# Performance work log

Measured on AMD Instinct MI355X. Metric: run time of the kernel, lower is better.

The kernel has to match this reference:

```python
import jax, jax.numpy as jnp
import numpy as np

C, HEADS, H, W = 256, 8, 64, 64
HD = C // HEADS
EPS = 1e-5

def conv1x1(x, w, b):
    # x:[B,C,H,W], w:[O,C], b:[O]
    return jnp.einsum('bchw,oc->bohw', x, w) + b[None, :, None, None]

def group_norm(x, scale, bias):
    B = x.shape[0]
    xg = x.reshape(B, HEADS, HD, H, W)
    mu = jnp.mean(xg, axis=(2, 3, 4), keepdims=True)
    var = jnp.var(xg, axis=(2, 3, 4), keepdims=True)
    xn = ((xg - mu) * jax.lax.rsqrt(var + EPS)).reshape(B, C, H, W)
    return xn * scale[None, :, None, None] + bias[None, :, None, None]

def setup_inputs() -> dict:
    key = jax.random.key(0)
    ks = jax.random.split(key, 12)
    s = 1.0 / np.sqrt(C)
    d = {
        'x': jax.random.normal(ks[0], (1, C, H, W), jnp.float32),
        'wq': jax.random.normal(ks[1], (C, C), jnp.float32) * s,
        'bq': jax.random.normal(ks[2], (C,), jnp.float32) * 0.01,
        'wk': jax.random.normal(ks[3], (C, C), jnp.float32) * s,
        'bk': jax.random.normal(ks[4], (C,), jnp.float32) * 0.01,
        'wv': jax.random.normal(ks[5], (C, C), jnp.float32) * s,
        'bv': jax.random.normal(ks[6], (C,), jnp.float32) * 0.01,
        'wo': jax.random.normal(ks[7], (C, C), jnp.float32) * s,
        'bo': jax.random.normal(ks[8], (C,), jnp.float32) * 0.01,
        'gn_scale': jnp.ones((C,), jnp.float32),
        'gn_bias': jnp.zeros((C,), jnp.float32),
        'gamma': jax.random.normal(ks[9], (1,), jnp.float32) * 0.1,
    }
    return d

def reference(x, wq, bq, wk, bk, wv, bv, wo, bo, gn_scale, gn_bias, gamma):
    B = x.shape[0]
    N = H * W
    scale = HD ** (-0.5)
    xn = group_norm(x, gn_scale, gn_bias)
    q = conv1x1(xn, wq, bq).reshape(B, HEADS, HD, N)
    k = conv1x1(xn, wk, bk).reshape(B, HEADS, HD, N)
    v = conv1x1(xn, wv, bv).reshape(B, HEADS, HD, N)
    attn = jnp.einsum('bhdn,bhdm->bhnm', q, k) * scale  # [B,h,N,N]
    attn = jax.nn.softmax(attn, axis=-1)
    out = jnp.einsum('bhnm,bhdm->bhdn', attn, v).reshape(B, C, H, W)
    out = conv1x1(out, wo, bo)
    return x + gamma * out
```

## Files before the change

kernel.cpp:

```cpp
#include <hip/hip_runtime.h>
#include <hip/hip_bf16.h>

#define C_DIM 256
#define N_SP  4096
#define HEADS 8
#define HD    32
#define GSIZE (HD * N_SP)

typedef __attribute__((ext_vector_type(8))) short bf16x8;
typedef __attribute__((ext_vector_type(4))) float f32x4;
typedef __attribute__((ext_vector_type(4))) unsigned u32x4;

__device__ inline unsigned short f2bf(float f) {
  unsigned int u = __builtin_bit_cast(unsigned int, f);
  u = (u + 0x7fffu + ((u >> 16) & 1u)) >> 16;
  return (unsigned short)u;
}
__device__ inline float bf2f(unsigned short b) {
  return __builtin_bit_cast(float, (unsigned)b << 16);
}

__device__ inline unsigned cvtpk_bf16(float lo, float hi) {
  unsigned r;
  asm("v_cvt_pk_bf16_f32 %0, %1, %2" : "=v"(r) : "v"(lo), "v"(hi));
  return r;
}
__device__ inline void pl32swap(unsigned &x, unsigned &y) {
  asm("v_permlane32_swap_b32 %0, %1" : "+v"(x), "+v"(y));
}
__device__ inline void pl16swap(unsigned &x, unsigned &y) {
  asm("v_permlane16_swap_b32 %0, %1" : "+v"(x), "+v"(y));
}
__device__ inline void gload_lds16(const void* g, void* l) {
  __builtin_amdgcn_global_load_lds(
      (const __attribute__((address_space(1))) void*)g,
      (__attribute__((address_space(3))) void*)l, 16, 0, 0);
}

__global__ __launch_bounds__(1024) void stats_cvt(const float* __restrict__ x,
                                                  float* __restrict__ stats,
                                                  const float* __restrict__ wq,
                                                  const float* __restrict__ wk,
                                                  const float* __restrict__ wv,
                                                  const float* __restrict__ wo,
                                                  unsigned short* __restrict__ dst) {
  int t = threadIdx.x;
  if (blockIdx.x < 8) {
    int g = blockIdx.x;
    const float4* xg = reinterpret_cast<const float4*>(x + (size_t)g * GSIZE);
    float s1 = 0.f, s2 = 0.f;
#pragma unroll
    for (int i = 0; i < 32; ++i) {
      float4 v = xg[t + i * 1024];
      s1 += v.x + v.y + v.z + v.w;
      s2 += v.x * v.x + v.y * v.y + v.z * v.z + v.w * v.w;
    }
    for (int off = 1; off < 64; off <<= 1) {
      s1 += __shfl_xor(s1, off);
      s2 += __shfl_xor(s2, off);
    }
    __shared__ float red[16][2];
    int wid = t >> 6;
    if ((t & 63) == 0) { red[wid][0] = s1; red[wid][1] = s2; }
    __syncthreads();
    if (t < 16) {
      s1 = red[t][0]; s2 = red[t][1];
      for (int off = 1; off < 16; off <<= 1) {
        s1 += __shfl_xor(s1, off);
        s2 += __shfl_xor(s2, off);
      }
      if (t == 0) {
        float mu = s1 / (float)GSIZE;
        float var = s2 / (float)GSIZE - mu * mu;
        stats[g * 2] = mu;
        stats[g * 2 + 1] = rsqrtf(var + 1e-5f);
      }
    }
  } else {
    int i = (blockIdx.x - 8) * 1024 + t;
    int mat = i >> 14;
    int idx = i & 16383;
    const float* src = (mat == 0) ? wq : (mat == 1) ? wk : (mat == 2) ? wv : wo;
    float4 v = reinterpret_cast<const float4*>(src)[idx];
    ushort4 o;
    o.x = f2bf(v.x); o.y = f2bf(v.y); o.z = f2bf(v.z); o.w = f2bf(v.w);
    reinterpret_cast<ushort4*>(dst + (size_t)mat * 65536)[idx] = o;
  }
}

__global__ __launch_bounds__(256) void gn_apply_t(const float* __restrict__ x,
                                                  const float* __restrict__ stats,
                                                  const float* __restrict__ gsc,
                                                  const float* __restrict__ gbi,
                                                  unsigned short* __restrict__ xnt) {
  __shared__ float tile[64][65];
  int t = threadIdx.x;
  int p0 = blockIdx.x * 64;
  int c0 = blockIdx.y * 64;
#pragma unroll
  for (int pass = 0; pass < 4; ++pass) {
    int f = t + pass * 256;
    int row = f >> 4, f4 = f & 15;
    int c = c0 + row;
    float4 v = *reinterpret_cast<const float4*>(x + (size_t)c * N_SP + p0 + f4 * 4);
    float mu = stats[(c >> 5) * 2], rs = stats[(c >> 5) * 2 + 1];
    float sc = gsc[c] * rs;
    float bi = gbi[c] - mu * sc;
    tile[row][f4 * 4 + 0] = v.x * sc + bi;
    tile[row][f4 * 4 + 1] = v.y * sc + bi;
    tile[row][f4 * 4 + 2] = v.z * sc + bi;
    tile[row][f4 * 4 + 3] = v.w * sc + bi;
  }
  __syncthreads();
#pragma unroll
  for (int pass = 0; pass < 4; ++pass) {
    int f = t + pass * 256;
    int p = f >> 4, cg = f & 15;
    ushort4 o;
    o.x = f2bf(tile[cg * 4 + 0][p]);
    o.y = f2bf(tile[cg * 4 + 1][p]);
    o.z = f2bf(tile[cg * 4 + 2][p]);
    o.w = f2bf(tile[cg * 4 + 3][p]);
    *reinterpret_cast<ushort4*>(xnt + (size_t)(p0 + p) * C_DIM + c0 + cg * 4) = o;
  }
}

__global__ __launch_bounds__(256) void gemm_qkv(const unsigned short* __restrict__ xnt,
                                                const unsigned short* __restrict__ wbf,
                                                const float* __restrict__ bq,
                                                const float* __restrict__ bk,
                                                const float* __restrict__ bv,
                                                unsigned short* __restrict__ qt,
                                                unsigned short* __restrict__ kt,
                                                unsigned short* __restrict__ vv) {
  int t = threadIdx.x;
  int w = t >> 6, lc = t & 15, lg = (t & 63) >> 4;
  int z = blockIdx.y;
  const unsigned short* Wb = wbf + (size_t)z * 65536;

  if (z < 2) {
    const float* bias = (z == 0) ? bq : bk;
    unsigned short* outt = (z == 0) ? qt : kt;
    float scale = (z == 0) ? 0.25503344494963116f : 1.0f;
    int n_base = (blockIdx.x >> 1) * 32 + (w >> 1) * 16;
    int o_base = (blockIdx.x & 1) * 128 + (w & 1) * 64;
    f32x4 acc[4];
#pragma unroll
    for (int ni = 0; ni < 4; ++ni) acc[ni] = (f32x4){0.f, 0.f, 0.f, 0.f};
#pragma unroll
    for (int c0 = 0; c0 < 256; c0 += 32) {
      bf16x8 a = *reinterpret_cast<const bf16x8*>(
          xnt + (size_t)(n_base + lc) * C_DIM + c0 + 8 * lg);
#pragma unroll
      for (int ni = 0; ni < 4; ++ni) {
        bf16x8 b = *reinterpret_cast<const bf16x8*>(
            Wb + (size_t)(o_base + 16 * ni + lc) * C_DIM + c0 + 8 * lg);
        acc[ni] = __builtin_amdgcn_mfma_f32_16x16x32_bf16(a, b, acc[ni], 0, 0, 0);
      }
    }
#pragma unroll
    for (int ni = 0; ni < 4; ++ni) {
      float bvv = bias[o_base + 16 * ni + lc];
#pragma unroll
      for (int r = 0; r < 4; ++r)
        outt[(size_t)(n_base + 4 * lg + r) * C_DIM + o_base + 16 * ni + lc] =
            f2bf((acc[ni][r] + bvv) * scale);
    }
  } else {
    int o_base = (blockIdx.x >> 6) * 64 + (w >> 1) * 32;
    int p_base = (blockIdx.x & 63) * 64 + (w & 1) * 32;
    f32x4 acc[2][2];
#pragma unroll
    for (int mi = 0; mi < 2; ++mi)
#pragma unroll
      for (int ni = 0; ni < 2; ++ni) acc[mi][ni] = (f32x4){0.f, 0.f, 0.f, 0.f};
#pragma unroll
    for (int c0 = 0; c0 < 256; c0 += 32) {
      bf16x8 a[2], b[2];
#pragma unroll
      for (int mi = 0; mi < 2; ++mi)
        a[mi] = *reinterpret_cast<const bf16x8*>(
            Wb + (size_t)(o_base + 16 * mi + lc) * C_DIM + c0 + 8 * lg);
#pragma unroll
      for (int ni = 0; ni < 2; ++ni)
        b[ni] = *reinterpret_cast<const bf16x8*>(
            xnt + (size_t)(p_base + 16 * ni + lc) * C_DIM + c0 + 8 * lg);
#pragma unroll
      for (int mi = 0; mi < 2; ++mi)
#pragma unroll
        for (int ni = 0; ni < 2; ++ni)
          acc[mi][ni] = __builtin_amdgcn_mfma_f32_16x16x32_bf16(a[mi], b[ni], acc[mi][ni], 0, 0, 0);
    }
#pragma unroll
    for (int mi = 0; mi < 2; ++mi)
#pragma unroll
      for (int r = 0; r < 4; ++r) {
        int o = o_base + 16 * mi + 4 * lg + r;
        float bvv = bv[o];
#pragma unroll
        for (int ni = 0; ni < 2; ++ni)
          vv[(size_t)o * N_SP + p_base + 16 * ni + lc] = f2bf(acc[mi][ni][r] + bvv);
      }
  }
}


#define STAGE_T(KB, VB, IT)                                                   \
  {                                                                           \
    gload_lds16(ksrc + (size_t)(IT) * 32768, smem + (KB) + w1024);            \
    gload_lds16(vsrc + (size_t)(IT) * 128, smem + (VB) + w1024);              \
  }

#define COMPUTE_TILE_L(KB, VB)                                                \
  {                                                                           \
    bf16x8 kf[4];                                                             \
    _Pragma("unroll")                                                         \
    for (int ni = 0; ni < 4; ++ni)                                            \
      kf[ni] = *reinterpret_cast<const bf16x8*>(smem + (KB) + ni * 1024 + krd); \
    bf16x8 vf[2][2];                                                          \
    _Pragma("unroll")                                                         \
    for (int dd = 0; dd < 2; ++dd) {                                          \
      vf[0][dd] = *reinterpret_cast<const bf16x8*>(smem + (VB) + dd * 2048 + vrd0); \
      vf[1][dd] = *reinterpret_cast<const bf16x8*>(smem + (VB) + dd * 2048 + vrd1); \
    }                                                                         \
    _Pragma("unroll")                                                         \
    for (int qi = 0; qi < 4; ++qi) {                                          \
      f32x4 s[4];                                                             \
      _Pragma("unroll")                                                       \
      for (int ni = 0; ni < 4; ++ni) {                                        \
        f32x4 z = (f32x4){0.f, 0.f, 0.f, 0.f};                                \
        s[ni] = __builtin_amdgcn_mfma_f32_16x16x32_bf16(kf[ni], qf[qi], z, 0, 0, 0); \
      }                                                                       \
      unsigned wd[4][2];                                                      \
      _Pragma("unroll")                                                       \
      for (int ni = 0; ni < 4; ++ni) {                                        \
        float p0 = __builtin_amdgcn_exp2f(s[ni][0]);                          \
        float p1 = __builtin_amdgcn_exp2f(s[ni][1]);                          \
        float p2 = __builtin_amdgcn_exp2f(s[ni][2]);                          \
        float p3 = __builtin_amdgcn_exp2f(s[ni][3]);                          \
        wd[ni][0] = cvtpk_bf16(p0, p1);                                       \
        wd[ni][1] = cvtpk_bf16(p2, p3);                                       \
      }                                                                       \
      bf16x8 ap[2];                                                           \
      _Pragma("unroll")                                                       \
      for (int kk = 0; kk < 2; ++kk) {                                        \
        unsigned a0 = wd[2 * kk][0], b0 = wd[2 * kk + 1][0];                  \
        unsigned a1 = wd[2 * kk][1], b1 = wd[2 * kk + 1][1];                  \
        pl32swap(a0, b0); pl16swap(a0, b0);                                   \
        pl32swap(a1, b1); pl16swap(a1, b1);                                   \
        u32x4 pk = {a0, a1, b0, b1};                                          \
        ap[kk] = __builtin_bit_cast(bf16x8, pk);                              \
      }                                                                       \
      lacc[qi] = __builtin_amdgcn_mfma_f32_16x16x32_bf16(ap[0], ones, lacc[qi], 0, 0, 0); \
      oacc[qi][0] = __builtin_amdgcn_mfma_f32_16x16x32_bf16(ap[0], vf[0][0], oacc[qi][0], 0, 0, 0); \
      oacc[qi][1] = __builtin_amdgcn_mfma_f32_16x16x32_bf16(ap[0], vf[0][1], oacc[qi][1], 0, 0, 0); \
      lacc[qi] = __builtin_amdgcn_mfma_f32_16x16x32_bf16(ap[1], ones, lacc[qi], 0, 0, 0); \
      oacc[qi][0] = __builtin_amdgcn_mfma_f32_16x16x32_bf16(ap[1], vf[1][0], oacc[qi][0], 0, 0, 0); \
      oacc[qi][1] = __builtin_amdgcn_mfma_f32_16x16x32_bf16(ap[1], vf[1][1], oacc[qi][1], 0, 0, 0); \
    }                                                                         \
  }

#define SYNC_T                                                                \
  {                                                                           \
    asm volatile("s_waitcnt vmcnt(0)" ::: "memory");                          \
    __syncthreads();                                                          \
  }

__global__ __launch_bounds__(256) void attn_part(const unsigned short* __restrict__ qt,
                                                 const unsigned short* __restrict__ kt,
                                                 const unsigned short* __restrict__ v,
                                                 unsigned short* __restrict__ po,
                                                 float* __restrict__ lp) {
  __shared__ __align__(1024) char smem[16384];
  int t = threadIdx.x;
  int w = t >> 6, lane = t & 63, lc = t & 15, lg = (t & 63) >> 4;
  int h = blockIdx.y, ks = blockIdx.z;
  int hc = h * HD;
  int nq0 = blockIdx.x * 256 + w * 64;
  int w1024 = w << 10;

  int kg = 64 * w + lane;
  int krow = kg >> 2;
  int kc16 = (kg & 3) ^ (krow & 3);
  const char* ksrc = (const char*)(kt + (size_t)(ks * 1024 + krow) * C_DIM + hc + 8 * kc16);
  int vg = 64 * w + lane;
  int vrow = vg >> 3;
  int vn16 = (vg & 7) ^ (vrow & 7);
  const char* vsrc = (const char*)(v + (size_t)(hc + vrow) * N_SP + ks * 1024 + 8 * vn16);

  int krd = lc * 64 + 16 * (lg ^ (lc & 3));
  int vrd0 = lc * 128 + 16 * ((lg + 0) ^ (lc & 7));
  int vrd1 = lc * 128 + 16 * ((lg + 4) ^ (lc & 7));

  bf16x8 qf[4];
#pragma unroll
  for (int qi = 0; qi < 4; ++qi)
    qf[qi] = *reinterpret_cast<const bf16x8*>(
        qt + (size_t)(nq0 + 16 * qi + lc) * C_DIM + hc + 8 * lg);

  f32x4 oacc[4][2], lacc[4];
#pragma unroll
  for (int qi = 0; qi < 4; ++qi) {
    lacc[qi] = (f32x4){0.f, 0.f, 0.f, 0.f};
#pragma unroll
    for (int dd = 0; dd < 2; ++dd) oacc[qi][dd] = (f32x4){0.f, 0.f, 0.f, 0.f};
  }
  const bf16x8 ones = {0x3F80, 0x3F80, 0x3F80, 0x3F80, 0x3F80, 0x3F80, 0x3F80, 0x3F80};

  STAGE_T(0, 8192, 0)
  SYNC_T
  for (int p = 0; p < 7; ++p) {
    STAGE_T(4096, 12288, 2 * p + 1)
    COMPUTE_TILE_L(0, 8192)
    SYNC_T
    STAGE_T(0, 8192, 2 * p + 2)
    COMPUTE_TILE_L(4096, 12288)
    SYNC_T
  }
  STAGE_T(4096, 12288, 15)
  COMPUTE_TILE_L(0, 8192)
  SYNC_T
  COMPUTE_TILE_L(4096, 12288)

  unsigned short* pob = po + (size_t)ks * (N_SP * C_DIM);
#pragma unroll
  for (int qi = 0; qi < 4; ++qi)
#pragma unroll
    for (int dd = 0; dd < 2; ++dd)
#pragma unroll
      for (int r = 0; r < 4; ++r)
        pob[(size_t)(nq0 + 16 * qi + 4 * lg + r) * C_DIM + hc + 16 * dd + lc] =
            f2bf(oacc[qi][dd][r]);
  if (lc == 0) {
#pragma unroll
    for (int qi = 0; qi < 4; ++qi)
#pragma unroll
      for (int r = 0; r < 4; ++r)
        lp[ks * 32768 + h * N_SP + nq0 + 16 * qi + 4 * lg + r] = lacc[qi][r];
  }
}

__global__ __launch_bounds__(256) void attn_merge(const unsigned short* __restrict__ po,
                                                  const float* __restrict__ lp,
                                                  unsigned short* __restrict__ aot) {
  int i = blockIdx.x * 256 + threadIdx.x;
  int n = i >> 5;
  int c0 = (i & 31) * 8;
  int h = c0 >> 5;
  float l = lp[h * N_SP + n] + lp[32768 + h * N_SP + n] +
            lp[65536 + h * N_SP + n] + lp[98304 + h * N_SP + n];
  float rl = 1.0f / l;
  float acc[8] = {0.f, 0.f, 0.f, 0.f, 0.f, 0.f, 0.f, 0.f};
#pragma unroll
  for (int ksplit = 0; ksplit < 4; ++ksplit) {
    bf16x8 vv = *reinterpret_cast<const bf16x8*>(po + (size_t)ksplit * (N_SP * C_DIM) + (size_t)i * 8);
#pragma unroll
    for (int j = 0; j < 8; ++j) acc[j] += bf2f((unsigned short)vv[j]);
  }
  bf16x8 o;
#pragma unroll
  for (int j = 0; j < 8; ++j) o[j] = (short)f2bf(acc[j] * rl);
  *reinterpret_cast<bf16x8*>(aot + (size_t)i * 8) = o;
}

__global__ __launch_bounds__(256) void gemm_out(const unsigned short* __restrict__ Wb,
                                                const unsigned short* __restrict__ aot,
                                                const float* __restrict__ bias,
                                                const float* __restrict__ x,
                                                const float* __restrict__ gamma,
                                                float* __restrict__ out) {
  int t = threadIdx.x;
  int w = t >> 6, lc = t & 15, lg = (t & 63) >> 4;
  int o_base = blockIdx.y * 64 + (w >> 1) * 32;
  int p_base = blockIdx.x * 64 + (w & 1) * 32;
  f32x4 acc[2][2];
#pragma unroll
  for (int mi = 0; mi < 2; ++mi)
#pragma unroll
    for (int ni = 0; ni < 2; ++ni) acc[mi][ni] = (f32x4){0.f, 0.f, 0.f, 0.f};
#pragma unroll
  for (int c0 = 0; c0 < 256; c0 += 32) {
    bf16x8 a[2], b[2];
#pragma unroll
    for (int mi = 0; mi < 2; ++mi)
      a[mi] = *reinterpret_cast<const bf16x8*>(
          Wb + (size_t)(o_base + 16 * mi + lc) * C_DIM + c0 + 8 * lg);
#pragma unroll
    for (int ni = 0; ni < 2; ++ni)
      b[ni] = *reinterpret_cast<const bf16x8*>(
          aot + (size_t)(p_base + 16 * ni + lc) * C_DIM + c0 + 8 * lg);
#pragma unroll
    for (int mi = 0; mi < 2; ++mi)
#pragma unroll
      for (int ni = 0; ni < 2; ++ni)
        acc[mi][ni] = __builtin_amdgcn_mfma_f32_16x16x32_bf16(a[mi], b[ni], acc[mi][ni], 0, 0, 0);
  }
  float g = gamma[0];
#pragma unroll
  for (int mi = 0; mi < 2; ++mi)
#pragma unroll
    for (int r = 0; r < 4; ++r) {
      int o = o_base + 16 * mi + 4 * lg + r;
      float bvv = bias[o];
#pragma unroll
      for (int ni = 0; ni < 2; ++ni) {
        size_t idx = (size_t)o * N_SP + p_base + 16 * ni + lc;
        out[idx] = x[idx] + g * (acc[mi][ni][r] + bvv);
      }
    }
}

extern "C" void kernel_launch(void* const* d_in, const int* in_sizes, int n_in,
                              void* d_out, int out_size, void* d_ws, size_t ws_size,
                              hipStream_t stream) {
  const float* x   = (const float*)d_in[0];
  const float* wq  = (const float*)d_in[1];
  const float* bq  = (const float*)d_in[2];
  const float* wk  = (const float*)d_in[3];
  const float* bk  = (const float*)d_in[4];
  const float* wv  = (const float*)d_in[5];
  const float* bv  = (const float*)d_in[6];
  const float* wo  = (const float*)d_in[7];
  const float* bo  = (const float*)d_in[8];
  const float* gsc = (const float*)d_in[9];
  const float* gbi = (const float*)d_in[10];
  const float* gamma = (const float*)d_in[11];
  float* out = (float*)d_out;

  char* ws = (char*)d_ws;
  float* stats          = (float*)ws;
  unsigned short* wbf   = (unsigned short*)(ws + 1024);
  unsigned short* qt    = (unsigned short*)(ws + 525312);
  unsigned short* kt    = (unsigned short*)(ws + 2622464);
  unsigned short* vv    = (unsigned short*)(ws + 4719616);
  unsigned short* aot   = (unsigned short*)(ws + 6816768);
  float* lp             = (float*)(ws + 8913920);
  unsigned short* xnt   = (unsigned short*)(ws + 9962496);
  unsigned short* po    = (unsigned short*)(ws + 12059648);

  stats_cvt<<<72, 1024, 0, stream>>>(x, stats, wq, wk, wv, wo, wbf);
  gn_apply_t<<<dim3(64, 4), 256, 0, stream>>>(x, stats, gsc, gbi, xnt);
  gemm_qkv<<<dim3(256, 3), 256, 0, stream>>>(xnt, wbf, bq, bk, bv, qt, kt, vv);
  attn_part<<<dim3(16, 8, 4), 256, 0, stream>>>(qt, kt, vv, po, lp);
  attn_merge<<<512, 256, 0, stream>>>(po, lp, aot);
  gemm_out<<<dim3(64, 4), 256, 0, stream>>>(wbf + 3 * 65536, aot, bo, x, gamma, out);
}
```

Measured before the change: 75.07 us.

## Double key tile per pipeline stage and interleave two independent MFMA chains

Each pipeline stage of the attention kernel now stages two 64-key K/V sub-tiles into a doubled 32 KB LDS buffer, which halves the number of barrier/waitcnt synchronisations per block. Inside each query sub-block it runs two independent score→exp→PV chains back to back so the scheduler can overlap MFMA latency with exp and permute work. Launch bounds now request 2 blocks per CU. In exchange the kernel uses more registers and LDS, which may reduce occupancy.

```diff
diff --git a/kernel.cpp b/kernel.cpp
--- a/kernel.cpp
+++ b/kernel.cpp
@@ -205,58 +205,69 @@
 }
 
 
-#define STAGE_T(KB, VB, IT)                                                   \
+#define STAGE_P(BB, IT)                                                       \
   {                                                                           \
-    gload_lds16(ksrc + (size_t)(IT) * 32768, smem + (KB) + w1024);            \
-    gload_lds16(vsrc + (size_t)(IT) * 128, smem + (VB) + w1024);              \
-  }
-
-#define COMPUTE_TILE_L(KB, VB)                                                \
+    gload_lds16(ksrc + (size_t)(IT) * 65536, smem + (BB) + w1024);            \
+    gload_lds16(ksrc + (size_t)(IT) * 65536 + 32768, smem + (BB) + 4096 + w1024); \
+    gload_lds16(vsrc + (size_t)(IT) * 256, smem + (BB) + 8192 + w1024);       \
+    gload_lds16(vsrc + (size_t)(IT) * 256 + 128, smem + (BB) + 12288 + w1024);\
+  }
+
+#define CHAIN(KF, VF)                                                         \
   {                                                                           \
-    bf16x8 kf[4];                                                             \
-    _Pragma("unroll")                                                         \
-    for (int ni = 0; ni < 4; ++ni)                                            \
-      kf[ni] = *reinterpret_cast<const bf16x8*>(smem + (KB) + ni * 1024 + krd); \
-    bf16x8 vf[2][2];                                                          \
+    f32x4 s[4];                                                               \
+    _Pragma("unroll")                                                         \
+    for (int ni = 0; ni < 4; ++ni) {                                          \
+      f32x4 z = (f32x4){0.f, 0.f, 0.f, 0.f};                                  \
+      s[ni] = __builtin_amdgcn_mfma_f32_16x16x32_bf16(KF[ni], qf[qi], z, 0, 0, 0); \
+    }                                                                         \
+    unsigned wd[4][2];                                                        \
+    _Pragma("unroll")                                                         \
+    for (int ni = 0; ni < 4; ++ni) {                                          \
+      float p0 = __builtin_amdgcn_exp2f(s[ni][0]);                            \
+      float p1 = __builtin_amdgcn_exp2f(s[ni][1]);                            \
+      float p2 = __builtin_amdgcn_exp2f(s[ni][2]);                            \
+      float p3 = __builtin_amdgcn_exp2f(s[ni][3]);                            \
+      wd[ni][0] = cvtpk_bf16(p0, p1);                                         \
+      wd[ni][1] = cvtpk_bf16(p2, p3);                                         \
+    }                                                                         \
+    bf16x8 ap[2];                                                             \
+    _Pragma("unroll")                                                         \
+    for (int kk = 0; kk < 2; ++kk) {                                          \
+      unsigned a0 = wd[2 * kk][0], b0 = wd[2 * kk + 1][0];                    \
+      unsigned a1 = wd[2 * kk][1], b1 = wd[2 * kk + 1][1];                    \
+      pl32swap(a0, b0); pl16swap(a0, b0);                                     \
+      pl32swap(a1, b1); pl16swap(a1, b1);                                     \
+      u32x4 pk = {a0, a1, b0, b1};                                            \
+      ap[kk] = __builtin_bit_cast(bf16x8, pk);                                \
+    }                                                                         \
+    lacc[qi] = __builtin_amdgcn_mfma_f32_16x16x32_bf16(ap[0], ones, lacc[qi], 0, 0, 0); \
+    oacc[qi][0] = __builtin_amdgcn_mfma_f32_16x16x32_bf16(ap[0], VF[0][0], oacc[qi][0], 0, 0, 0); \
+    oacc[qi][1] = __builtin_amdgcn_mfma_f32_16x16x32_bf16(ap[0], VF[0][1], oacc[qi][1], 0, 0, 0); \
+    lacc[qi] = __builtin_amdgcn_mfma_f32_16x16x32_bf16(ap[1], ones, lacc[qi], 0, 0, 0); \
+    oacc[qi][0] = __builtin_amdgcn_mfma_f32_16x16x32_bf16(ap[1], VF[1][0], oacc[qi][0], 0, 0, 0); \
+    oacc[qi][1] = __builtin_amdgcn_mfma_f32_16x16x32_bf16(ap[1], VF[1][1], oacc[qi][1], 0, 0, 0); \
+  }
+
+#define COMPUTE_P(BB)                                                         \
+  {                                                                           \
+    bf16x8 kf0[4], kf1[4], vf0[2][2], vf1[2][2];                              \
+    _Pragma("unroll")                                                         \
+    for (int ni = 0; ni < 4; ++ni) {                                          \
+      kf0[ni] = *reinterpret_cast<const bf16x8*>(smem + (BB) + ni * 1024 + krd); \
+      kf1[ni] = *reinterpret_cast<const bf16x8*>(smem + (BB) + 4096 + ni * 1024 + krd); \
+    }                                                                         \
     _Pragma("unroll")                                                         \
     for (int dd = 0; dd < 2; ++dd) {                                          \
-      vf[0][dd] = *reinterpret_cast<const bf16x8*>(smem + (VB) + dd * 2048 + vrd0); \
-      vf[1][dd] = *reinterpret_cast<const bf16x8*>(smem + (VB) + dd * 2048 + vrd1); \
+      vf0[0][dd] = *reinterpret_cast<const bf16x8*>(smem + (BB) + 8192 + dd * 2048 + vrd0); \
+      vf0[1][dd] = *reinterpret_cast<const bf16x8*>(smem + (BB) + 8192 + dd * 2048 + vrd1); \
+      vf1[0][dd] = *reinterpret_cast<const bf16x8*>(smem + (BB) + 12288 + dd * 2048 + vrd0); \
+      vf1[1][dd] = *reinterpret_cast<const bf16x8*>(smem + (BB) + 12288 + dd * 2048 + vrd1); \
     }                                                                         \
     _Pragma("unroll")                                                         \
     for (int qi = 0; qi < 4; ++qi) {                                          \
-      f32x4 s[4];                                                             \
-      _Pragma("unroll")                                                       \
-      for (int ni = 0; ni < 4; ++ni) {                                        \
-        f32x4 z = (f32x4){0.f, 0.f, 0.f, 0.f};                                \
-        s[ni] = __builtin_amdgcn_mfma_f32_16x16x32_bf16(kf[ni], qf[qi], z, 0, 0, 0); \
-      }                                                                       \
-      unsigned wd[4][2];                                                      \
-      _Pragma("unroll")                                                       \
-      for (int ni = 0; ni < 4; ++ni) {                                        \
-        float p0 = __builtin_amdgcn_exp2f(s[ni][0]);                          \
-        float p1 = __builtin_amdgcn_exp2f(s[ni][1]);                          \
-        float p2 = __builtin_amdgcn_exp2f(s[ni][2]);                          \
-        float p3 = __builtin_amdgcn_exp2f(s[ni][3]);                          \
-        wd[ni][0] = cvtpk_bf16(p0, p1);                                       \
-        wd[ni][1] = cvtpk_bf16(p2, p3);                                       \
-      }                                                                       \
-      bf16x8 ap[2];                                                           \
-      _Pragma("unroll")                                                       \
-      for (int kk = 0; kk < 2; ++kk) {                                        \
-        unsigned a0 = wd[2 * kk][0], b0 = wd[2 * kk + 1][0];                  \
-        unsigned a1 = wd[2 * kk][1], b1 = wd[2 * kk + 1][1];                  \
-        pl32swap(a0, b0); pl16swap(a0, b0);                                   \
-        pl32swap(a1, b1); pl16swap(a1, b1);                                   \
-        u32x4 pk = {a0, a1, b0, b1};                                          \
-        ap[kk] = __builtin_bit_cast(bf16x8, pk);                              \
-      }                                                                       \
-      lacc[qi] = __builtin_amdgcn_mfma_f32_16x16x32_bf16(ap[0], ones, lacc[qi], 0, 0, 0); \
-      oacc[qi][0] = __builtin_amdgcn_mfma_f32_16x16x32_bf16(ap[0], vf[0][0], oacc[qi][0], 0, 0, 0); \
-      oacc[qi][1] = __builtin_amdgcn_mfma_f32_16x16x32_bf16(ap[0], vf[0][1], oacc[qi][1], 0, 0, 0); \
-      lacc[qi] = __builtin_amdgcn_mfma_f32_16x16x32_bf16(ap[1], ones, lacc[qi], 0, 0, 0); \
-      oacc[qi][0] = __builtin_amdgcn_mfma_f32_16x16x32_bf16(ap[1], vf[1][0], oacc[qi][0], 0, 0, 0); \
-      oacc[qi][1] = __builtin_amdgcn_mfma_f32_16x16x32_bf16(ap[1], vf[1][1], oacc[qi][1], 0, 0, 0); \
+      CHAIN(kf0, vf0)                                                         \
+      CHAIN(kf1, vf1)                                                         \
     }                                                                         \
   }
 
@@ -266,12 +277,12 @@
     __syncthreads();                                                          \
   }
 
-__global__ __launch_bounds__(256) void attn_part(const unsigned short* __restrict__ qt,
-                                                 const unsigned short* __restrict__ kt,
-                                                 const unsigned short* __restrict__ v,
-                                                 unsigned short* __restrict__ po,
-                                                 float* __restrict__ lp) {
-  __shared__ __align__(1024) char smem[16384];
+__global__ __launch_bounds__(256, 2) void attn_part(const unsigned short* __restrict__ qt,
+                                                    const unsigned short* __restrict__ kt,
+                                                    const unsigned short* __restrict__ v,
+                                                    unsigned short* __restrict__ po,
+                                                    float* __restrict__ lp) {
+  __shared__ __align__(1024) char smem[32768];
   int t = threadIdx.x;
   int w = t >> 6, lane = t & 63, lc = t & 15, lg = (t & 63) >> 4;
   int h = blockIdx.y, ks = blockIdx.z;
@@ -307,20 +318,20 @@
   }
   const bf16x8 ones = {0x3F80, 0x3F80, 0x3F80, 0x3F80, 0x3F80, 0x3F80, 0x3F80, 0x3F80};
 
-  STAGE_T(0, 8192, 0)
+  STAGE_P(0, 0)
   SYNC_T
-  for (int p = 0; p < 7; ++p) {
-    STAGE_T(4096, 12288, 2 * p + 1)
-    COMPUTE_TILE_L(0, 8192)
+  for (int p = 0; p < 3; ++p) {
+    STAGE_P(16384, 2 * p + 1)
+    COMPUTE_P(0)
     SYNC_T
-    STAGE_T(0, 8192, 2 * p + 2)
-    COMPUTE_TILE_L(4096, 12288)
+    STAGE_P(0, 2 * p + 2)
+    COMPUTE_P(16384)
     SYNC_T
   }
-  STAGE_T(4096, 12288, 15)
-  COMPUTE_TILE_L(0, 8192)
+  STAGE_P(16384, 7)
+  COMPUTE_P(0)
   SYNC_T
-  COMPUTE_TILE_L(4096, 12288)
+  COMPUTE_P(16384)
 
   unsigned short* pob = po + (size_t)ks * (N_SP * C_DIM);
 #pragma unroll
```

After: 68.98 us. -8.1%, faster.
